# Kernel optimization log

Hardware: AMD Instinct MI355X
Metric: run time of the kernel (lower is better)

## Reference

```python
import jax, jax.numpy as jnp
import numpy as np

B, K, L, P = 8192, 25, 25, 1
BN_EPS = 1e-5


def setup_inputs() -> dict:
    key = jax.random.key(0)
    ks = jax.random.split(key, 12)
    s = 0.3  # weight init scale
    return {
        "x": jax.random.normal(ks[0], (B, L), dtype=jnp.float32),
        "gamma": jnp.ones((L,), dtype=jnp.float32),
        "bn_bias": jnp.zeros((L,), dtype=jnp.float32),
        "W1": s * jax.random.normal(ks[1], (K, L, P, 8), dtype=jnp.float32),
        "b1": s * jax.random.normal(ks[2], (K, L, P, 8), dtype=jnp.float32),
        "W2": s * jax.random.normal(ks[3], (K, L, P, 8, 8), dtype=jnp.float32),
        "b2": s * jax.random.normal(ks[4], (K, L, P, 8), dtype=jnp.float32),
        "W3": s * jax.random.normal(ks[5], (K, L, P, 6, 8), dtype=jnp.float32),
        "b3": s * jax.random.normal(ks[6], (K, L, P, 6), dtype=jnp.float32),
        "W4": s * jax.random.normal(ks[7], (K, L, P, 6), dtype=jnp.float32),
        "b4": s * jax.random.normal(ks[8], (K, L, P), dtype=jnp.float32),
        "alpha": jax.random.uniform(ks[9], (L, K), dtype=jnp.float32),
        "beta": jax.random.normal(ks[10], (K,), dtype=jnp.float32),
    }


def reference(x, gamma, bn_bias, W1, b1, W2, b2, W3, b3, W4, b4, alpha, beta):
    # BatchNorm1d(L) in training mode: biased batch statistics over the batch dim
    mean = jnp.mean(x, axis=0)
    var = jnp.var(x, axis=0)
    xn = (x - mean) * jax.lax.rsqrt(var + BN_EPS) * gamma + bn_bias  # [B, L]

    # Batched tiny MLPs: one 1->8->8->6->1 net per (k, l, p)
    h1 = jax.nn.relu(jnp.einsum('bl,klph->bklph', xn, W1) + b1)          # [B,K,L,P,8]
    h2 = jax.nn.relu(jnp.einsum('bklph,klpih->bklpi', h1, W2) + b2)      # [B,K,L,P,8]
    h3 = jax.nn.relu(jnp.einsum('bklpi,klpji->bklpj', h2, W3) + b3)      # [B,K,L,P,6]
    f = jnp.einsum('bklpj,klpj->bklp', h3, W4) + b4                      # [B,K,L,P]
    out = jnp.swapaxes(jnp.sum(f, axis=-1), 1, 2)                        # [B,L,K] (sum over p)
    return beta + jnp.sum(out * alpha[None, :, :], axis=1)               # [B,K]
```

## Files before the change

kernel.cpp:

```cpp
#include <hip/hip_runtime.h>

#define BATCH  8192
#define KK     25
#define LL     25
#define BN_EPS 1e-5f
#define PREPB  32
#define LG     5
#define NLG    (LL / LG)
#define VB     4

#define WS_PART   0
#define WS_SCALE  1600
#define WS_SHIFT  1632
#define WS_XT     2048
#define WS_FP     (WS_XT + LL * BATCH)
#define WS_END    (WS_FP + NLG * KK * BATCH)

__global__ __launch_bounds__(256) void prep_kernel(
    const float* __restrict__ x,
    float* __restrict__ xT,
    float* __restrict__ part)
{
    __shared__ float xs[256 * LL];
    const int tid = threadIdx.x;
    const int b0  = blockIdx.x * 256;

    const float* src = x + (size_t)b0 * LL;
    #pragma unroll
    for (int i = 0; i < LL; ++i)
        xs[i * 256 + tid] = src[i * 256 + tid];
    __syncthreads();

    #pragma unroll
    for (int l = 0; l < LL; ++l)
        xT[l * BATCH + b0 + tid] = xs[tid * LL + l];

    float s = 0.f, s2 = 0.f;
    if (tid < 200) {
        const int l = tid % LL;
        const int g = tid / LL;
        #pragma unroll
        for (int r = 0; r < 32; ++r) {
            const float v = xs[(g * 32 + r) * LL + l];
            s += v;
            s2 = fmaf(v, v, s2);
        }
    }
    __syncthreads();
    if (tid < 200) { xs[tid] = s; xs[200 + tid] = s2; }
    __syncthreads();

    if (tid < 50) {
        const int c = tid;
        float t = 0.f;
        if (c < LL) {
            #pragma unroll
            for (int g = 0; g < 8; ++g) t += xs[g * LL + c];
        } else {
            #pragma unroll
            for (int g = 0; g < 8; ++g) t += xs[200 + g * LL + (c - LL)];
        }
        part[blockIdx.x * 50 + c] = t;
    }
}

__global__ __launch_bounds__(64) void stats2_kernel(
    const float* __restrict__ part,
    const float* __restrict__ gamma,
    const float* __restrict__ bn_bias,
    float* __restrict__ ws)
{
    const int c = threadIdx.x;
    float t = 0.f;
    if (c < 50)
        for (int b = 0; b < PREPB; ++b)
            t += part[b * 50 + c];

    const int src = (c < LL) ? (c + LL) : c;
    const float s2 = __shfl(t, src);

    if (c < LL) {
        const float inv_b = 1.f / (float)BATCH;
        const float mean  = t * inv_b;
        const float var   = fmaf(s2, inv_b, -mean * mean);
        const float scale = rsqrtf(var + BN_EPS) * gamma[c];
        ws[WS_SCALE + c] = scale;
        ws[WS_SHIFT + c] = fmaf(-mean, scale, bn_bias[c]);
    }
}

__global__ __launch_bounds__(256) void eval_kernel(
    const float* __restrict__ xT,
    const float* __restrict__ W1, const float* __restrict__ b1,
    const float* __restrict__ W2, const float* __restrict__ b2,
    const float* __restrict__ W3, const float* __restrict__ b3,
    const float* __restrict__ W4, const float* __restrict__ b4,
    const float* __restrict__ alpha,
    const float* __restrict__ ws,
    float* __restrict__ fp)
{
    const int tid = threadIdx.x;
    const int k   = blockIdx.y;
    const int g   = blockIdx.z;
    const int b   = (blockIdx.x * 256 + tid) * VB;
    const int l0  = g * LG;

    float acc[VB] = {0.f, 0.f, 0.f, 0.f};

    for (int j = 0; j < LG; ++j) {
        const int l  = l0 + j;
        const int kl = k * LL + l;
        const float scale = ws[WS_SCALE + l];
        const float shift = ws[WS_SHIFT + l];

        const float4 xv = *(const float4*)&xT[l * BATCH + b];
        float xn[VB] = {
            fmaf(xv.x, scale, shift), fmaf(xv.y, scale, shift),
            fmaf(xv.z, scale, shift), fmaf(xv.w, scale, shift)
        };

        const float* w1  = W1 + kl * 8;
        const float* bb1 = b1 + kl * 8;
        float h1[VB][8];
        #pragma unroll
        for (int h = 0; h < 8; ++h) {
            const float w = w1[h], bb = bb1[h];
            #pragma unroll
            for (int v = 0; v < VB; ++v)
                h1[v][h] = fmaxf(fmaf(xn[v], w, bb), 0.f);
        }

        const float* w2  = W2 + kl * 64;
        const float* bb2 = b2 + kl * 8;
        float h2[VB][8];
        #pragma unroll
        for (int i = 0; i < 8; ++i) {
            const float bb = bb2[i];
            float t[VB] = {bb, bb, bb, bb};
            #pragma unroll
            for (int h = 0; h < 8; ++h) {
                const float w = w2[i * 8 + h];
                #pragma unroll
                for (int v = 0; v < VB; ++v)
                    t[v] = fmaf(h1[v][h], w, t[v]);
            }
            #pragma unroll
            for (int v = 0; v < VB; ++v)
                h2[v][i] = fmaxf(t[v], 0.f);
        }

        const float* w3  = W3 + kl * 48;
        const float* bb3 = b3 + kl * 6;
        float h3[VB][6];
        #pragma unroll
        for (int jj = 0; jj < 6; ++jj) {
            const float bb = bb3[jj];
            float t[VB] = {bb, bb, bb, bb};
            #pragma unroll
            for (int i = 0; i < 8; ++i) {
                const float w = w3[jj * 8 + i];
                #pragma unroll
                for (int v = 0; v < VB; ++v)
                    t[v] = fmaf(h2[v][i], w, t[v]);
            }
            #pragma unroll
            for (int v = 0; v < VB; ++v)
                h3[v][jj] = fmaxf(t[v], 0.f);
        }

        const float* w4 = W4 + kl * 6;
        const float b4v = b4[kl];
        const float a   = alpha[l * KK + k];
        #pragma unroll
        for (int v = 0; v < VB; ++v) {
            float f = b4v;
            #pragma unroll
            for (int jj = 0; jj < 6; ++jj)
                f = fmaf(h3[v][jj], w4[jj], f);
            acc[v] = fmaf(a, f, acc[v]);
        }
    }

    float4 o = {acc[0], acc[1], acc[2], acc[3]};
    *(float4*)&fp[(g * KK + k) * BATCH + b] = o;
}

__global__ __launch_bounds__(256) void reduce_kernel(
    const float* __restrict__ fp,
    const float* __restrict__ beta,
    float* __restrict__ out)
{
    const int tid = threadIdx.x;
    const int k   = blockIdx.y;
    const int b   = blockIdx.x * 256 + tid;

    float acc = beta[k];
    #pragma unroll
    for (int g = 0; g < NLG; ++g)
        acc += fp[(g * KK + k) * BATCH + b];
    out[(size_t)b * KK + k] = acc;
}

__device__ __forceinline__ float mlp_eval(
    float xn, int kl,
    const float* __restrict__ W1, const float* __restrict__ b1,
    const float* __restrict__ W2, const float* __restrict__ b2,
    const float* __restrict__ W3, const float* __restrict__ b3,
    const float* __restrict__ W4, const float* __restrict__ b4)
{
    const float* w1  = W1 + kl * 8;
    const float* bb1 = b1 + kl * 8;
    float h1[8];
    #pragma unroll
    for (int h = 0; h < 8; ++h)
        h1[h] = fmaxf(fmaf(xn, w1[h], bb1[h]), 0.f);

    const float* w2  = W2 + kl * 64;
    const float* bb2 = b2 + kl * 8;
    float h2[8];
    #pragma unroll
    for (int i = 0; i < 8; ++i) {
        float t = bb2[i];
        #pragma unroll
        for (int h = 0; h < 8; ++h)
            t = fmaf(h1[h], w2[i * 8 + h], t);
        h2[i] = fmaxf(t, 0.f);
    }

    const float* w3  = W3 + kl * 48;
    const float* bb3 = b3 + kl * 6;
    float h3[6];
    #pragma unroll
    for (int j = 0; j < 6; ++j) {
        float t = bb3[j];
        #pragma unroll
        for (int i = 0; i < 8; ++i)
            t = fmaf(h2[i], w3[j * 8 + i], t);
        h3[j] = fmaxf(t, 0.f);
    }

    const float* w4 = W4 + kl * 6;
    float f = b4[kl];
    #pragma unroll
    for (int j = 0; j < 6; ++j)
        f = fmaf(h3[j], w4[j], f);
    return f;
}

__global__ __launch_bounds__(256) void stats_small_kernel(
    const float* __restrict__ x,
    const float* __restrict__ gamma,
    const float* __restrict__ bn_bias,
    float* __restrict__ ws)
{
    const int l   = blockIdx.x;
    const int tid = threadIdx.x;

    float s = 0.f, s2 = 0.f;
    for (int b = tid; b < BATCH; b += 256) {
        float v = x[b * LL + l];
        s  += v;
        s2  = fmaf(v, v, s2);
    }
    for (int off = 32; off > 0; off >>= 1) {
        s  += __shfl_down(s,  off);
        s2 += __shfl_down(s2, off);
    }
    __shared__ float red[8];
    const int wave = tid >> 6;
    if ((tid & 63) == 0) { red[wave] = s; red[4 + wave] = s2; }
    __syncthreads();
    if (tid == 0) {
        s  = red[0] + red[1] + red[2] + red[3];
        s2 = red[4] + red[5] + red[6] + red[7];
        const float inv_b = 1.f / (float)BATCH;
        float mean = s * inv_b;
        float var  = fmaf(s2, inv_b, -mean * mean);
        float scale = rsqrtf(var + BN_EPS) * gamma[l];
        ws[WS_SCALE + l] = scale;
        ws[WS_SHIFT + l] = fmaf(-mean, scale, bn_bias[l]);
    }
}

__global__ __launch_bounds__(256) void mlp_lds_direct_kernel(
    const float* __restrict__ x,
    const float* __restrict__ W1, const float* __restrict__ b1,
    const float* __restrict__ W2, const float* __restrict__ b2,
    const float* __restrict__ W3, const float* __restrict__ b3,
    const float* __restrict__ W4, const float* __restrict__ b4,
    const float* __restrict__ alpha, const float* __restrict__ beta,
    const float* __restrict__ ws,
    float* __restrict__ out)
{
    __shared__ float xs[256 * LL];
    const int tid = threadIdx.x;
    const int k   = blockIdx.y;
    const int b0  = blockIdx.x * 256;

    const float* xsrc = x + (size_t)b0 * LL;
    #pragma unroll
    for (int i = 0; i < LL; ++i)
        xs[i * 256 + tid] = xsrc[i * 256 + tid];
    __syncthreads();

    float acc = beta[k];
    for (int l = 0; l < LL; ++l) {
        const int kl = k * LL + l;
        const float xn = fmaf(xs[tid * LL + l], ws[WS_SCALE + l], ws[WS_SHIFT + l]);
        const float f  = mlp_eval(xn, kl, W1, b1, W2, b2, W3, b3, W4, b4);
        acc = fmaf(alpha[l * KK + k], f, acc);
    }
    out[(size_t)(b0 + tid) * KK + k] = acc;
}

extern "C" void kernel_launch(void* const* d_in, const int* in_sizes, int n_in,
                              void* d_out, int out_size, void* d_ws, size_t ws_size,
                              hipStream_t stream) {
    const float* x       = (const float*)d_in[0];
    const float* gamma   = (const float*)d_in[1];
    const float* bn_bias = (const float*)d_in[2];
    const float* W1      = (const float*)d_in[3];
    const float* b1      = (const float*)d_in[4];
    const float* W2      = (const float*)d_in[5];
    const float* b2      = (const float*)d_in[6];
    const float* W3      = (const float*)d_in[7];
    const float* b3      = (const float*)d_in[8];
    const float* W4      = (const float*)d_in[9];
    const float* b4      = (const float*)d_in[10];
    const float* alpha   = (const float*)d_in[11];
    const float* beta    = (const float*)d_in[12];

    float* out = (float*)d_out;
    float* ws  = (float*)d_ws;
    float* xT  = ws + WS_XT;
    float* fp  = ws + WS_FP;

    const bool fast = ws_size >= (size_t)WS_END * sizeof(float);

    if (fast) {
        prep_kernel<<<dim3(PREPB), dim3(256), 0, stream>>>(x, xT, ws + WS_PART);
        stats2_kernel<<<dim3(1), dim3(64), 0, stream>>>(ws + WS_PART, gamma, bn_bias, ws);
        eval_kernel<<<dim3(BATCH / (256 * VB), KK, NLG), dim3(256), 0, stream>>>(
            xT, W1, b1, W2, b2, W3, b3, W4, b4, alpha, ws, fp);
        reduce_kernel<<<dim3(BATCH / 256, KK), dim3(256), 0, stream>>>(fp, beta, out);
    } else {
        stats_small_kernel<<<dim3(LL), dim3(256), 0, stream>>>(x, gamma, bn_bias, ws);
        mlp_lds_direct_kernel<<<dim3(BATCH / 256, KK), dim3(256), 0, stream>>>(
            x, W1, b1, W2, b2, W3, b3, W4, b4, alpha, beta, ws, out);
    }
}
```

Measured before the change: 113.2 us.

## Fuse BN stats finalize into eval kernel and stage MLP weights in LDS

Removes the single-block stats2 kernel launch; each eval block now reduces the per-block partial sums for its own five features and computes the scale and shift itself. Each block also copies the weights for its five (k,l) MLPs into shared memory before computing, so the inner loops read LDS instead of issuing scalar global loads. It also unrolls the l loop and adds a min-blocks-per-CU hint to launch bounds. The cost is redundant stats reduction in every block, extra barriers, and higher register pressure from the unroll.

```diff
diff --git a/kernel.cpp b/kernel.cpp
--- a/kernel.cpp
+++ b/kernel.cpp
@@ -8,6 +8,7 @@
 #define LG     5
 #define NLG    (LL / LG)
 #define VB     4
+#define WSTRIDE 160
 
 #define WS_PART   0
 #define WS_SCALE  1600
@@ -64,119 +65,144 @@
     }
 }
 
-__global__ __launch_bounds__(64) void stats2_kernel(
-    const float* __restrict__ part,
-    const float* __restrict__ gamma,
-    const float* __restrict__ bn_bias,
-    float* __restrict__ ws)
-{
-    const int c = threadIdx.x;
-    float t = 0.f;
-    if (c < 50)
-        for (int b = 0; b < PREPB; ++b)
-            t += part[b * 50 + c];
-
-    const int src = (c < LL) ? (c + LL) : c;
-    const float s2 = __shfl(t, src);
-
-    if (c < LL) {
-        const float inv_b = 1.f / (float)BATCH;
-        const float mean  = t * inv_b;
-        const float var   = fmaf(s2, inv_b, -mean * mean);
-        const float scale = rsqrtf(var + BN_EPS) * gamma[c];
-        ws[WS_SCALE + c] = scale;
-        ws[WS_SHIFT + c] = fmaf(-mean, scale, bn_bias[c]);
-    }
-}
-
-__global__ __launch_bounds__(256) void eval_kernel(
+__global__ __launch_bounds__(256, 3) void eval_kernel(
     const float* __restrict__ xT,
     const float* __restrict__ W1, const float* __restrict__ b1,
     const float* __restrict__ W2, const float* __restrict__ b2,
     const float* __restrict__ W3, const float* __restrict__ b3,
     const float* __restrict__ W4, const float* __restrict__ b4,
     const float* __restrict__ alpha,
-    const float* __restrict__ ws,
+    const float* __restrict__ part,
+    const float* __restrict__ gamma,
+    const float* __restrict__ bn_bias,
     float* __restrict__ fp)
 {
+    __shared__ float wl[LG * WSTRIDE];
+    __shared__ float tmp[2 * LG];
+
     const int tid = threadIdx.x;
     const int k   = blockIdx.y;
     const int g   = blockIdx.z;
+    const int l0  = g * LG;
+    const int kl0 = k * LL + l0;
     const int b   = (blockIdx.x * 256 + tid) * VB;
-    const int l0  = g * LG;
+
+    if (tid < 40) {
+        const int j = tid >> 3, e = tid & 7;
+        wl[j * WSTRIDE +      e] = W1[(kl0 + j) * 8 + e];
+        wl[j * WSTRIDE +  8 + e] = b1[(kl0 + j) * 8 + e];
+        wl[j * WSTRIDE + 80 + e] = b2[(kl0 + j) * 8 + e];
+    }
+    {
+        int t = tid;
+        const int j = t >> 6, e = t & 63;
+        wl[j * WSTRIDE + 16 + e] = W2[(kl0 + j) * 64 + e];
+        t += 256;
+        if (t < LG * 64) {
+            const int j2 = t >> 6, e2 = t & 63;
+            wl[j2 * WSTRIDE + 16 + e2] = W2[(kl0 + j2) * 64 + e2];
+        }
+    }
+    if (tid < 240) {
+        const int j = tid / 48, e = tid % 48;
+        wl[j * WSTRIDE + 88 + e] = W3[(kl0 + j) * 48 + e];
+    }
+    if (tid < 30) {
+        const int j = tid / 6, e = tid % 6;
+        wl[j * WSTRIDE + 136 + e] = b3[(kl0 + j) * 6 + e];
+        wl[j * WSTRIDE + 142 + e] = W4[(kl0 + j) * 6 + e];
+    }
+    if (tid < LG) {
+        wl[tid * WSTRIDE + 148] = b4[kl0 + tid];
+        wl[tid * WSTRIDE + 149] = alpha[(l0 + tid) * KK + k];
+    }
+
+    if (tid >= 128 && tid < 128 + 2 * LG) {
+        const int t2  = tid - 128;
+        const int col = (t2 < LG) ? (l0 + t2) : (LL + l0 + t2 - LG);
+        float s = 0.f;
+        #pragma unroll
+        for (int i = 0; i < PREPB; ++i)
+            s += part[i * 50 + col];
+        tmp[t2] = s;
+    }
+    __syncthreads();
+    if (tid < LG) {
+        const float s = tmp[tid], s2 = tmp[LG + tid];
+        const float inv_b = 1.f / (float)BATCH;
+        const float mean  = s * inv_b;
+        const float var   = fmaf(s2, inv_b, -mean * mean);
+        const float scale = rsqrtf(var + BN_EPS) * gamma[l0 + tid];
+        wl[tid * WSTRIDE + 150] = scale;
+        wl[tid * WSTRIDE + 151] = fmaf(-mean, scale, bn_bias[l0 + tid]);
+    }
+    __syncthreads();
 
     float acc[VB] = {0.f, 0.f, 0.f, 0.f};
 
+    #pragma unroll
     for (int j = 0; j < LG; ++j) {
-        const int l  = l0 + j;
-        const int kl = k * LL + l;
-        const float scale = ws[WS_SCALE + l];
-        const float shift = ws[WS_SHIFT + l];
-
-        const float4 xv = *(const float4*)&xT[l * BATCH + b];
+        const float* w = wl + j * WSTRIDE;
+        const float scale = w[150];
+        const float shift = w[151];
+
+        const float4 xv = *(const float4*)&xT[(l0 + j) * BATCH + b];
         float xn[VB] = {
             fmaf(xv.x, scale, shift), fmaf(xv.y, scale, shift),
             fmaf(xv.z, scale, shift), fmaf(xv.w, scale, shift)
         };
 
-        const float* w1  = W1 + kl * 8;
-        const float* bb1 = b1 + kl * 8;
         float h1[VB][8];
         #pragma unroll
         for (int h = 0; h < 8; ++h) {
-            const float w = w1[h], bb = bb1[h];
+            const float ww = w[h], bb = w[8 + h];
             #pragma unroll
             for (int v = 0; v < VB; ++v)
-                h1[v][h] = fmaxf(fmaf(xn[v], w, bb), 0.f);
-        }
-
-        const float* w2  = W2 + kl * 64;
-        const float* bb2 = b2 + kl * 8;
+                h1[v][h] = fmaxf(fmaf(xn[v], ww, bb), 0.f);
+        }
+
         float h2[VB][8];
         #pragma unroll
         for (int i = 0; i < 8; ++i) {
-            const float bb = bb2[i];
+            const float bb = w[80 + i];
             float t[VB] = {bb, bb, bb, bb};
             #pragma unroll
             for (int h = 0; h < 8; ++h) {
-                const float w = w2[i * 8 + h];
+                const float ww = w[16 + i * 8 + h];
                 #pragma unroll
                 for (int v = 0; v < VB; ++v)
-                    t[v] = fmaf(h1[v][h], w, t[v]);
+                    t[v] = fmaf(h1[v][h], ww, t[v]);
             }
             #pragma unroll
             for (int v = 0; v < VB; ++v)
                 h2[v][i] = fmaxf(t[v], 0.f);
         }
 
-        const float* w3  = W3 + kl * 48;
-        const float* bb3 = b3 + kl * 6;
         float h3[VB][6];
         #pragma unroll
         for (int jj = 0; jj < 6; ++jj) {
-            const float bb = bb3[jj];
+            const float bb = w[136 + jj];
             float t[VB] = {bb, bb, bb, bb};
             #pragma unroll
             for (int i = 0; i < 8; ++i) {
-                const float w = w3[jj * 8 + i];
+                const float ww = w[88 + jj * 8 + i];
                 #pragma unroll
                 for (int v = 0; v < VB; ++v)
-                    t[v] = fmaf(h2[v][i], w, t[v]);
+                    t[v] = fmaf(h2[v][i], ww, t[v]);
             }
             #pragma unroll
             for (int v = 0; v < VB; ++v)
                 h3[v][jj] = fmaxf(t[v], 0.f);
         }
 
-        const float* w4 = W4 + kl * 6;
-        const float b4v = b4[kl];
-        const float a   = alpha[l * KK + k];
+        const float b4v = w[148];
+        const float a   = w[149];
         #pragma unroll
         for (int v = 0; v < VB; ++v) {
             float f = b4v;
             #pragma unroll
             for (int jj = 0; jj < 6; ++jj)
-                f = fmaf(h3[v][jj], w4[jj], f);
+                f = fmaf(h3[v][jj], w[142 + jj], f);
             acc[v] = fmaf(a, f, acc[v]);
         }
     }
@@ -339,9 +365,9 @@
 
     if (fast) {
         prep_kernel<<<dim3(PREPB), dim3(256), 0, stream>>>(x, xT, ws + WS_PART);
-        stats2_kernel<<<dim3(1), dim3(64), 0, stream>>>(ws + WS_PART, gamma, bn_bias, ws);
         eval_kernel<<<dim3(BATCH / (256 * VB), KK, NLG), dim3(256), 0, stream>>>(
-            xT, W1, b1, W2, b2, W3, b3, W4, b4, alpha, ws, fp);
+            xT, W1, b1, W2, b2, W3, b3, W4, b4, alpha,
+            ws + WS_PART, gamma, bn_bias, fp);
         reduce_kernel<<<dim3(BATCH / 256, KK), dim3(256), 0, stream>>>(fp, beta, out);
     } else {
         stats_small_kernel<<<dim3(LL), dim3(256), 0, stream>>>(x, gamma, bn_bias, ws);
```

New measurement: 102.2 us. 1.11x faster.

## Evaluate MLP layers in packed fp16 with LDS-staged weights; shrink prep blocks

Applied to the files above, without the earlier changes.

The eval kernel now converts each block's weights to packed half2 values in shared memory and runs all MLP layers with packed fp16 FMAs on pairs of batch elements. Only the final per-(k,l) value is accumulated in fp32. This aims to double arithmetic throughput on the compute-bound tiny-MLP work and replace repeated scalar weight loads with LDS reads. The prep kernel is also restructured into 128 blocks of 64 rows to increase parallelism. The cost is reduced precision from fp16 intermediates, which may exceed tolerance.

```diff
diff --git a/kernel.cpp b/kernel.cpp
--- a/kernel.cpp
+++ b/kernel.cpp
@@ -4,50 +4,69 @@
 #define KK     25
 #define LL     25
 #define BN_EPS 1e-5f
-#define PREPB  32
+#define PREPB  128
 #define LG     5
 #define NLG    (LL / LG)
 #define VB     4
+#define WS2    152
 
 #define WS_PART   0
-#define WS_SCALE  1600
-#define WS_SHIFT  1632
-#define WS_XT     2048
+#define WS_SCALE  6400
+#define WS_SHIFT  6432
+#define WS_XT     8192
 #define WS_FP     (WS_XT + LL * BATCH)
 #define WS_END    (WS_FP + NLG * KK * BATCH)
+
+typedef _Float16 h2 __attribute__((ext_vector_type(2)));
+
+static __device__ __forceinline__ h2 bcast2(float w) {
+    const _Float16 h = (_Float16)w;
+    h2 r; r.x = h; r.y = h; return r;
+}
+static __device__ __forceinline__ h2 relu2(h2 v) {
+    h2 z; z.x = (_Float16)0.f; z.y = (_Float16)0.f;
+    return __builtin_elementwise_max(v, z);
+}
 
 __global__ __launch_bounds__(256) void prep_kernel(
     const float* __restrict__ x,
     float* __restrict__ xT,
     float* __restrict__ part)
 {
-    __shared__ float xs[256 * LL];
+    __shared__ float xs[64 * LL];
+    __shared__ float red[400];
     const int tid = threadIdx.x;
-    const int b0  = blockIdx.x * 256;
+    const int b0  = blockIdx.x * 64;
 
     const float* src = x + (size_t)b0 * LL;
     #pragma unroll
-    for (int i = 0; i < LL; ++i)
-        xs[i * 256 + tid] = src[i * 256 + tid];
+    for (int i = 0; i < 7; ++i) {
+        const int idx = i * 256 + tid;
+        if (idx < 64 * LL) xs[idx] = src[idx];
+    }
     __syncthreads();
 
     #pragma unroll
-    for (int l = 0; l < LL; ++l)
-        xT[l * BATCH + b0 + tid] = xs[tid * LL + l];
+    for (int i = 0; i < 7; ++i) {
+        const int idx = i * 256 + tid;
+        if (idx < 64 * LL) {
+            const int l = idx >> 6, r = idx & 63;
+            xT[l * BATCH + b0 + r] = xs[r * LL + l];
+        }
+    }
 
     float s = 0.f, s2 = 0.f;
     if (tid < 200) {
         const int l = tid % LL;
         const int g = tid / LL;
         #pragma unroll
-        for (int r = 0; r < 32; ++r) {
-            const float v = xs[(g * 32 + r) * LL + l];
+        for (int r = 0; r < 8; ++r) {
+            const float v = xs[(g * 8 + r) * LL + l];
             s += v;
             s2 = fmaf(v, v, s2);
         }
-    }
-    __syncthreads();
-    if (tid < 200) { xs[tid] = s; xs[200 + tid] = s2; }
+        red[tid] = s; red[200 + tid] = s2;
+    }
     __syncthreads();
 
     if (tid < 50) {
@@ -55,10 +74,10 @@
         float t = 0.f;
         if (c < LL) {
             #pragma unroll
-            for (int g = 0; g < 8; ++g) t += xs[g * LL + c];
+            for (int g = 0; g < 8; ++g) t += red[g * LL + c];
         } else {
             #pragma unroll
-            for (int g = 0; g < 8; ++g) t += xs[200 + g * LL + (c - LL)];
+            for (int g = 0; g < 8; ++g) t += red[200 + g * LL + (c - LL)];
         }
         part[blockIdx.x * 50 + c] = t;
     }
@@ -99,86 +118,117 @@
     const float* __restrict__ ws,
     float* __restrict__ fp)
 {
+    __shared__ h2 wl[LG * WS2];
+
     const int tid = threadIdx.x;
     const int k   = blockIdx.y;
     const int g   = blockIdx.z;
+    const int l0  = g * LG;
+    const int kl0 = k * LL + l0;
     const int b   = (blockIdx.x * 256 + tid) * VB;
-    const int l0  = g * LG;
+
+    if (tid < 40) {
+        const int j = tid >> 3, e = tid & 7;
+        wl[j * WS2 +      e] = bcast2(W1[(kl0 + j) * 8 + e]);
+        wl[j * WS2 +  8 + e] = bcast2(b1[(kl0 + j) * 8 + e]);
+        wl[j * WS2 + 80 + e] = bcast2(b2[(kl0 + j) * 8 + e]);
+    }
+    {
+        int t = tid;
+        const int j = t >> 6, e = t & 63;
+        wl[j * WS2 + 16 + e] = bcast2(W2[(kl0 + j) * 64 + e]);
+        t += 256;
+        if (t < LG * 64) {
+            const int j2 = t >> 6, e2 = t & 63;
+            wl[j2 * WS2 + 16 + e2] = bcast2(W2[(kl0 + j2) * 64 + e2]);
+        }
+    }
+    if (tid < 240) {
+        const int j = tid / 48, e = tid % 48;
+        wl[j * WS2 + 88 + e] = bcast2(W3[(kl0 + j) * 48 + e]);
+    }
+    if (tid < 30) {
+        const int j = tid / 6, e = tid % 6;
+        wl[j * WS2 + 136 + e] = bcast2(b3[(kl0 + j) * 6 + e]);
+        wl[j * WS2 + 142 + e] = bcast2(W4[(kl0 + j) * 6 + e]);
+    }
+    __syncthreads();
 
     float acc[VB] = {0.f, 0.f, 0.f, 0.f};
 
+    #pragma unroll
     for (int j = 0; j < LG; ++j) {
-        const int l  = l0 + j;
-        const int kl = k * LL + l;
+        const int l = l0 + j;
+        const h2* w = wl + j * WS2;
+
         const float scale = ws[WS_SCALE + l];
         const float shift = ws[WS_SHIFT + l];
+        const float a     = alpha[l * KK + k];
+        const float b4f   = b4[kl0 + j];
 
         const float4 xv = *(const float4*)&xT[l * BATCH + b];
-        float xn[VB] = {
-            fmaf(xv.x, scale, shift), fmaf(xv.y, scale, shift),
-            fmaf(xv.z, scale, shift), fmaf(xv.w, scale, shift)
-        };
-
-        const float* w1  = W1 + kl * 8;
-        const float* bb1 = b1 + kl * 8;
-        float h1[VB][8];
+        h2 xn2[2];
+        {
+            const float n0 = fmaf(xv.x, scale, shift);
+            const float n1 = fmaf(xv.y, scale, shift);
+            const float n2 = fmaf(xv.z, scale, shift);
+            const float n3 = fmaf(xv.w, scale, shift);
+            xn2[0].x = (_Float16)n0; xn2[0].y = (_Float16)n1;
+            xn2[1].x = (_Float16)n2; xn2[1].y = (_Float16)n3;
+        }
+
+        h2 hh1[2][8];
         #pragma unroll
         for (int h = 0; h < 8; ++h) {
-            const float w = w1[h], bb = bb1[h];
+            const h2 ww = w[h], bb = w[8 + h];
             #pragma unroll
-            for (int v = 0; v < VB; ++v)
-                h1[v][h] = fmaxf(fmaf(xn[v], w, bb), 0.f);
-        }
-
-        const float* w2  = W2 + kl * 64;
-        const float* bb2 = b2 + kl * 8;
-        float h2[VB][8];
+            for (int p = 0; p < 2; ++p)
+                hh1[p][h] = relu2(xn2[p] * ww + bb);
+        }
+
+        h2 hh2[2][8];
         #pragma unroll
         for (int i = 0; i < 8; ++i) {
-            const float bb = bb2[i];
-            float t[VB] = {bb, bb, bb, bb};
+            const h2 bb = w[80 + i];
+            h2 t0 = bb, t1 = bb;
             #pragma unroll
             for (int h = 0; h < 8; ++h) {
-                const float w = w2[i * 8 + h];
-                #pragma unroll
-                for (int v = 0; v < VB; ++v)
-                    t[v] = fmaf(h1[v][h], w, t[v]);
+                const h2 ww = w[16 + i * 8 + h];
+                t0 = hh1[0][h] * ww + t0;
+                t1 = hh1[1][h] * ww + t1;
             }
-            #pragma unroll
-            for (int v = 0; v < VB; ++v)
-                h2[v][i] = fmaxf(t[v], 0.f);
-        }
-
-        const float* w3  = W3 + kl * 48;
-        const float* bb3 = b3 + kl * 6;
-        float h3[VB][6];
+            hh2[0][i] = relu2(t0);
+            hh2[1][i] = relu2(t1);
+        }
+
+        h2 hh3[2][6];
         #pragma unroll
         for (int jj = 0; jj < 6; ++jj) {
-            const float bb = bb3[jj];
-            float t[VB] = {bb, bb, bb, bb};
+            const h2 bb = w[136 + jj];
+            h2 t0 = bb, t1 = bb;
             #pragma unroll
             for (int i = 0; i < 8; ++i) {
-                const float w = w3[jj * 8 + i];
-                #pragma unroll
-                for (int v = 0; v < VB; ++v)
-                    t[v] = fmaf(h2[v][i], w, t[v]);
+                const h2 ww = w[88 + jj * 8 + i];
+                t0 = hh2[0][i] * ww + t0;
+                t1 = hh2[1][i] * ww + t1;
             }
-            #pragma unroll
-            for (int v = 0; v < VB; ++v)
-                h3[v][jj] = fmaxf(t[v], 0.f);
-        }
-
-        const float* w4 = W4 + kl * 6;
-        const float b4v = b4[kl];
-        const float a   = alpha[l * KK + k];
-        #pragma unroll
-        for (int v = 0; v < VB; ++v) {
-            float f = b4v;
-            #pragma unroll
-            for (int jj = 0; jj < 6; ++jj)
-                f = fmaf(h3[v][jj], w4[jj], f);
-            acc[v] = fmaf(a, f, acc[v]);
-        }
+            hh3[0][jj] = relu2(t0);
+            hh3[1][jj] = relu2(t1);
+        }
+
+        h2 fd0, fd1;
+        fd0.x = (_Float16)0.f; fd0.y = (_Float16)0.f;
+        fd1 = fd0;
+        #pragma unroll
+        for (int jj = 0; jj < 6; ++jj) {
+            const h2 ww = w[142 + jj];
+            fd0 = hh3[0][jj] * ww + fd0;
+            fd1 = hh3[1][jj] * ww + fd1;
+        }
+        acc[0] = fmaf(a, b4f + (float)fd0.x, acc[0]);
+        acc[1] = fmaf(a, b4f + (float)fd0.y, acc[1]);
+        acc[2] = fmaf(a, b4f + (float)fd1.x, acc[2]);
+        acc[3] = fmaf(a, b4f + (float)fd1.y, acc[3]);
     }
 
     float4 o = {acc[0], acc[1], acc[2], acc[3]};
@@ -217,14 +267,14 @@
 
     const float* w2  = W2 + kl * 64;
     const float* bb2 = b2 + kl * 8;
-    float h2[8];
+    float h2v[8];
     #pragma unroll
     for (int i = 0; i < 8; ++i) {
         float t = bb2[i];
         #pragma unroll
         for (int h = 0; h < 8; ++h)
             t = fmaf(h1[h], w2[i * 8 + h], t);
-        h2[i] = fmaxf(t, 0.f);
+        h2v[i] = fmaxf(t, 0.f);
     }
 
     const float* w3  = W3 + kl * 48;
@@ -235,7 +285,7 @@
         float t = bb3[j];
         #pragma unroll
         for (int i = 0; i < 8; ++i)
-            t = fmaf(h2[i], w3[j * 8 + i], t);
+            t = fmaf(h2v[i], w3[j * 8 + i], t);
         h3[j] = fmaxf(t, 0.f);
     }
 
```

Result: faster. 104.5 us (-7.8%).
